# Optimization experiments

Measured on AMD Instinct MI355X. Metric: run time of the kernel, lower is better.

The kernel has to match this reference:

```python
import jax, jax.numpy as jnp
import numpy as np
from jax import lax

# Dims fixed by the module: Linear(96,24) => 16 channels * (24/4) length => per-step feature L=24
L = 24

def _conv1d(x, w, b):
    # x: (N, Cin, L), w: (Cout, Cin, K), 'same' padding for K=3
    y = lax.conv_general_dilated(x, w, window_strides=(1,), padding=[(1, 1)],
                                 dimension_numbers=("NCH", "OIH", "NCH"))
    return y + b[None, :, None]

def _maxpool2(x):
    # x: (N, C, L) -> (N, C, L//2), non-overlapping window of 2
    n, c, l = x.shape
    return x.reshape(n, c, l // 2, 2).max(axis=-1)

def setup_inputs() -> dict:
    key = jax.random.key(0)
    ks = jax.random.split(key, 11)
    S, B = 512, 256
    def u(k, shape, fan_in):
        bound = 1.0 / np.sqrt(fan_in)
        return jax.random.uniform(k, shape, jnp.float32, -bound, bound)
    return {
        "x":   jax.random.normal(ks[0], (S, B, L), jnp.float32),
        "w11": u(ks[1], (8, 1, 3), 1 * 3),   "b11": u(ks[2], (8,), 1 * 3),
        "w12": u(ks[3], (8, 8, 3), 8 * 3),   "b12": u(ks[4], (8,), 8 * 3),
        "w21": u(ks[5], (16, 8, 3), 8 * 3),  "b21": u(ks[6], (16,), 8 * 3),
        "w22": u(ks[7], (16, 16, 3), 16 * 3), "b22": u(ks[8], (16,), 16 * 3),
        "Wl":  u(ks[9], (24, 96), 96),        "bl": u(ks[10], (24,), 96),
    }

def reference(x, w11, b11, w12, b12, w21, b21, w22, b22, Wl, bl):
    # Original loops over timesteps applying the same CNN; timestep and batch
    # are independent, so fuse them into one conv batch (identical math).
    S, B, Lf = x.shape
    h = x.reshape(S * B, 1, Lf)                 # (SB, 1, 24)
    h = jax.nn.relu(_conv1d(h, w11, b11))       # (SB, 8, 24); Dropout(0.1) = identity in eval
    h = jax.nn.relu(_conv1d(h, w12, b12))       # (SB, 8, 24)
    h = _maxpool2(h)                            # (SB, 8, 12)
    h = jax.nn.relu(_conv1d(h, w21, b21))       # (SB, 16, 12); Dropout = identity in eval
    h = jax.nn.relu(_conv1d(h, w22, b22))       # (SB, 16, 12)
    h = _maxpool2(h)                            # (SB, 16, 6)
    h = h.reshape(S, B, 96)                     # torch reshape(batch, -1) per step
    return h @ Wl.T + bl                        # (S, B, 24)
```

## Files before the change

### kernel.cpp

```cpp
#include <hip/hip_runtime.h>


#define TPB 256

__launch_bounds__(TPB, 2)
__global__ void cnn_pre_lstm_kernel(
    const float* __restrict__ x,
    const float* __restrict__ w11, const float* __restrict__ b11,
    const float* __restrict__ w12, const float* __restrict__ b12,
    const float* __restrict__ w21, const float* __restrict__ b21,
    const float* __restrict__ w22, const float* __restrict__ b22,
    const float* __restrict__ Wl,  const float* __restrict__ bl,
    float* __restrict__ out)
{
    __shared__ float sA[12288];
    __shared__ float sB[6144];

    const int tid = threadIdx.x;
    const int ln  = tid & 63;
    const int wv  = __builtin_amdgcn_readfirstlane(tid >> 6);

    {
        const float* xg = x + (size_t)blockIdx.x * (64 * 24);
        #pragma unroll
        for (int k = 0; k < 6; ++k) {
            int o = tid + k * TPB;
            int s = o / 24, p = o % 24;
            sB[s * 25 + p] = xg[o];
        }
    }
    __syncthreads();

    {
        const int co0 = wv * 2;
        float wA0 = w11[co0*3+0], wA1 = w11[co0*3+1], wA2 = w11[co0*3+2];
        float wB0 = w11[(co0+1)*3+0], wB1 = w11[(co0+1)*3+1], wB2 = w11[(co0+1)*3+2];
        float bA = b11[co0], bB = b11[co0+1];

        float xm = 0.f, xc = sB[ln*25 + 0], xp;
        #pragma unroll
        for (int p = 0; p < 24; ++p) {
            xp = (p < 23) ? sB[ln*25 + p + 1] : 0.f;
            float a = fmaf(wA0, xm, fmaf(wA1, xc, fmaf(wA2, xp, bA)));
            float b = fmaf(wB0, xm, fmaf(wB1, xc, fmaf(wB2, xp, bB)));
            sA[ co0      * 1536 + p * 64 + ln] = fmaxf(a, 0.f);
            sA[(co0 + 1) * 1536 + p * 64 + ln] = fmaxf(b, 0.f);
            xm = xc; xc = xp;
        }
    }
    __syncthreads();

    {
        const int co0 = wv * 2;
        float acc[2][24];
        #pragma unroll
        for (int i = 0; i < 2; ++i) {
            float bb = b12[co0 + i];
            #pragma unroll
            for (int p = 0; p < 24; ++p) acc[i][p] = bb;
        }
        for (int ci = 0; ci < 8; ++ci) {
            float wg[2][3];
            #pragma unroll
            for (int i = 0; i < 2; ++i) {
                const float* wp = w12 + ((co0 + i) * 8 + ci) * 3;
                wg[i][0] = wp[0]; wg[i][1] = wp[1]; wg[i][2] = wp[2];
            }
            const int cb = ci * 1536 + ln;
            float xm = 0.f, xc = sA[cb], xp;
            #pragma unroll
            for (int p = 0; p < 24; ++p) {
                xp = (p < 23) ? sA[cb + (p + 1) * 64] : 0.f;
                #pragma unroll
                for (int i = 0; i < 2; ++i)
                    acc[i][p] = fmaf(wg[i][0], xm, fmaf(wg[i][1], xc, fmaf(wg[i][2], xp, acc[i][p])));
                xm = xc; xc = xp;
            }
        }
        #pragma unroll
        for (int i = 0; i < 2; ++i)
            #pragma unroll
            for (int p2 = 0; p2 < 12; ++p2)
                sB[(co0 + i) * 768 + p2 * 64 + ln] =
                    fmaxf(fmaxf(acc[i][2*p2], acc[i][2*p2+1]), 0.f);
    }
    __syncthreads();

    {
        const int co0 = wv * 4;
        float acc[4][12];
        #pragma unroll
        for (int i = 0; i < 4; ++i) {
            float bb = b21[co0 + i];
            #pragma unroll
            for (int p = 0; p < 12; ++p) acc[i][p] = bb;
        }
        for (int ci = 0; ci < 8; ++ci) {
            float wg[4][3];
            #pragma unroll
            for (int i = 0; i < 4; ++i) {
                const float* wp = w21 + ((co0 + i) * 8 + ci) * 3;
                wg[i][0] = wp[0]; wg[i][1] = wp[1]; wg[i][2] = wp[2];
            }
            const int cb = ci * 768 + ln;
            float xm = 0.f, xc = sB[cb], xp;
            #pragma unroll
            for (int p = 0; p < 12; ++p) {
                xp = (p < 11) ? sB[cb + (p + 1) * 64] : 0.f;
                #pragma unroll
                for (int i = 0; i < 4; ++i)
                    acc[i][p] = fmaf(wg[i][0], xm, fmaf(wg[i][1], xc, fmaf(wg[i][2], xp, acc[i][p])));
                xm = xc; xc = xp;
            }
        }
        #pragma unroll
        for (int i = 0; i < 4; ++i)
            #pragma unroll
            for (int p = 0; p < 12; ++p)
                sA[(co0 + i) * 768 + p * 64 + ln] = fmaxf(acc[i][p], 0.f);
    }
    __syncthreads();

    {
        const int co0 = wv * 4;
        float acc[4][12];
        #pragma unroll
        for (int i = 0; i < 4; ++i) {
            float bb = b22[co0 + i];
            #pragma unroll
            for (int p = 0; p < 12; ++p) acc[i][p] = bb;
        }
        for (int ci = 0; ci < 16; ++ci) {
            float wg[4][3];
            #pragma unroll
            for (int i = 0; i < 4; ++i) {
                const float* wp = w22 + ((co0 + i) * 16 + ci) * 3;
                wg[i][0] = wp[0]; wg[i][1] = wp[1]; wg[i][2] = wp[2];
            }
            const int cb = ci * 768 + ln;
            float xm = 0.f, xc = sA[cb], xp;
            #pragma unroll
            for (int p = 0; p < 12; ++p) {
                xp = (p < 11) ? sA[cb + (p + 1) * 64] : 0.f;
                #pragma unroll
                for (int i = 0; i < 4; ++i)
                    acc[i][p] = fmaf(wg[i][0], xm, fmaf(wg[i][1], xc, fmaf(wg[i][2], xp, acc[i][p])));
                xm = xc; xc = xp;
            }
        }
        #pragma unroll
        for (int i = 0; i < 4; ++i)
            #pragma unroll
            for (int p2 = 0; p2 < 6; ++p2)
                sB[(co0 + i) * 384 + p2 * 64 + ln] =
                    fmaxf(fmaxf(acc[i][2*p2], acc[i][2*p2+1]), 0.f);
    }
    __syncthreads();

    {
        const int j0 = wv * 6;
        float acc6[6];
        #pragma unroll
        for (int i = 0; i < 6; ++i) acc6[i] = bl[j0 + i];
        for (int c = 0; c < 16; ++c) {
            #pragma unroll
            for (int p = 0; p < 6; ++p) {
                float v = sB[c * 384 + p * 64 + ln];
                const int f = c * 6 + p;
                #pragma unroll
                for (int i = 0; i < 6; ++i)
                    acc6[i] = fmaf(Wl[(j0 + i) * 96 + f], v, acc6[i]);
            }
        }
        #pragma unroll
        for (int i = 0; i < 6; ++i)
            sA[ln * 24 + j0 + i] = acc6[i];
    }
    __syncthreads();

    {
        float* og = out + (size_t)blockIdx.x * (64 * 24);
        #pragma unroll
        for (int k = 0; k < 6; ++k) {
            int o = tid + k * TPB;
            og[o] = sA[o];
        }
    }
}

extern "C" void kernel_launch(void* const* d_in, const int* in_sizes, int n_in,
                              void* d_out, int out_size, void* d_ws, size_t ws_size,
                              hipStream_t stream) {
    const float* x   = (const float*)d_in[0];
    const float* w11 = (const float*)d_in[1];
    const float* b11 = (const float*)d_in[2];
    const float* w12 = (const float*)d_in[3];
    const float* b12 = (const float*)d_in[4];
    const float* w21 = (const float*)d_in[5];
    const float* b21 = (const float*)d_in[6];
    const float* w22 = (const float*)d_in[7];
    const float* b22 = (const float*)d_in[8];
    const float* Wl  = (const float*)d_in[9];
    const float* bl  = (const float*)d_in[10];
    float* out = (float*)d_out;

    const int n_samples = in_sizes[0] / 24;
    const int blocks = n_samples / 64;

    hipLaunchKernelGGL(cnn_pre_lstm_kernel, dim3(blocks), dim3(TPB), 0, stream,
                       x, w11, b11, w12, b12, w21, b21, w22, b22, Wl, bl, out);
}
```

Measured before the change: 163.6 us.

## Use 512-thread blocks with one output channel per wave and padded output staging

Doubles the block to 8 waves, so each wave computes half as many output channels per conv stage and half as many linear outputs. This raises parallelism and cuts per-thread register and accumulator pressure, and the launch bound now asks for 4 blocks per CU. The output staging buffer is padded to a stride of 25 to avoid LDS bank conflicts on the final write. In exchange each wave now reloads the shared input rows for fewer outputs, which adds LDS read traffic, and the large per-block LDS footprint may limit how many blocks actually fit on a CU.

New measurement: 164.1 us. No clear change (+0.3%).

```diff
diff --git a/kernel.cpp b/kernel.cpp
--- a/kernel.cpp
+++ b/kernel.cpp
@@ -1,9 +1,9 @@
 #include <hip/hip_runtime.h>
 
 
-#define TPB 256
-
-__launch_bounds__(TPB, 2)
+#define TPB 512
+
+__launch_bounds__(TPB, 4)
 __global__ void cnn_pre_lstm_kernel(
     const float* __restrict__ x,
     const float* __restrict__ w11, const float* __restrict__ b11,
@@ -23,7 +23,7 @@
     {
         const float* xg = x + (size_t)blockIdx.x * (64 * 24);
         #pragma unroll
-        for (int k = 0; k < 6; ++k) {
+        for (int k = 0; k < 3; ++k) {
             int o = tid + k * TPB;
             int s = o / 24, p = o % 24;
             sB[s * 25 + p] = xg[o];
@@ -32,45 +32,69 @@
     __syncthreads();
 
     {
-        const int co0 = wv * 2;
-        float wA0 = w11[co0*3+0], wA1 = w11[co0*3+1], wA2 = w11[co0*3+2];
-        float wB0 = w11[(co0+1)*3+0], wB1 = w11[(co0+1)*3+1], wB2 = w11[(co0+1)*3+2];
-        float bA = b11[co0], bB = b11[co0+1];
+        const int co = wv;
+        float w0 = w11[co*3+0], w1 = w11[co*3+1], w2 = w11[co*3+2];
+        float bb = b11[co];
 
         float xm = 0.f, xc = sB[ln*25 + 0], xp;
         #pragma unroll
         for (int p = 0; p < 24; ++p) {
             xp = (p < 23) ? sB[ln*25 + p + 1] : 0.f;
-            float a = fmaf(wA0, xm, fmaf(wA1, xc, fmaf(wA2, xp, bA)));
-            float b = fmaf(wB0, xm, fmaf(wB1, xc, fmaf(wB2, xp, bB)));
-            sA[ co0      * 1536 + p * 64 + ln] = fmaxf(a, 0.f);
-            sA[(co0 + 1) * 1536 + p * 64 + ln] = fmaxf(b, 0.f);
+            float a = fmaf(w0, xm, fmaf(w1, xc, fmaf(w2, xp, bb)));
+            sA[co * 1536 + p * 64 + ln] = fmaxf(a, 0.f);
             xm = xc; xc = xp;
         }
     }
     __syncthreads();
 
     {
+        const int co = wv;
+        float acc[24];
+        {
+            float bb = b12[co];
+            #pragma unroll
+            for (int p = 0; p < 24; ++p) acc[p] = bb;
+        }
+        for (int ci = 0; ci < 8; ++ci) {
+            const float* wp = w12 + (co * 8 + ci) * 3;
+            float w0 = wp[0], w1 = wp[1], w2 = wp[2];
+            const int cb = ci * 1536 + ln;
+            float xm = 0.f, xc = sA[cb], xp;
+            #pragma unroll
+            for (int p = 0; p < 24; ++p) {
+                xp = (p < 23) ? sA[cb + (p + 1) * 64] : 0.f;
+                acc[p] = fmaf(w0, xm, fmaf(w1, xc, fmaf(w2, xp, acc[p])));
+                xm = xc; xc = xp;
+            }
+        }
+        #pragma unroll
+        for (int q = 0; q < 12; ++q)
+            sB[co * 768 + q * 64 + ln] =
+                fmaxf(fmaxf(acc[2*q], acc[2*q+1]), 0.f);
+    }
+    __syncthreads();
+
+    {
         const int co0 = wv * 2;
-        float acc[2][24];
+        float acc[2][12];
         #pragma unroll
         for (int i = 0; i < 2; ++i) {
-            float bb = b12[co0 + i];
-            #pragma unroll
-            for (int p = 0; p < 24; ++p) acc[i][p] = bb;
+            float bb = b21[co0 + i];
+            #pragma unroll
+            for (int p = 0; p < 12; ++p) acc[i][p] = bb;
         }
         for (int ci = 0; ci < 8; ++ci) {
             float wg[2][3];
             #pragma unroll
             for (int i = 0; i < 2; ++i) {
-                const float* wp = w12 + ((co0 + i) * 8 + ci) * 3;
+                const float* wp = w21 + ((co0 + i) * 8 + ci) * 3;
                 wg[i][0] = wp[0]; wg[i][1] = wp[1]; wg[i][2] = wp[2];
             }
-            const int cb = ci * 1536 + ln;
-            float xm = 0.f, xc = sA[cb], xp;
-            #pragma unroll
-            for (int p = 0; p < 24; ++p) {
-                xp = (p < 23) ? sA[cb + (p + 1) * 64] : 0.f;
+            const int cb = ci * 768 + ln;
+            float xm = 0.f, xc = sB[cb], xp;
+            #pragma unroll
+            for (int p = 0; p < 12; ++p) {
+                xp = (p < 11) ? sB[cb + (p + 1) * 64] : 0.f;
                 #pragma unroll
                 for (int i = 0; i < 2; ++i)
                     acc[i][p] = fmaf(wg[i][0], xm, fmaf(wg[i][1], xc, fmaf(wg[i][2], xp, acc[i][p])));
@@ -80,60 +104,24 @@
         #pragma unroll
         for (int i = 0; i < 2; ++i)
             #pragma unroll
-            for (int p2 = 0; p2 < 12; ++p2)
-                sB[(co0 + i) * 768 + p2 * 64 + ln] =
-                    fmaxf(fmaxf(acc[i][2*p2], acc[i][2*p2+1]), 0.f);
-    }
-    __syncthreads();
-
-    {
-        const int co0 = wv * 4;
-        float acc[4][12];
-        #pragma unroll
-        for (int i = 0; i < 4; ++i) {
-            float bb = b21[co0 + i];
-            #pragma unroll
-            for (int p = 0; p < 12; ++p) acc[i][p] = bb;
-        }
-        for (int ci = 0; ci < 8; ++ci) {
-            float wg[4][3];
-            #pragma unroll
-            for (int i = 0; i < 4; ++i) {
-                const float* wp = w21 + ((co0 + i) * 8 + ci) * 3;
-                wg[i][0] = wp[0]; wg[i][1] = wp[1]; wg[i][2] = wp[2];
-            }
-            const int cb = ci * 768 + ln;
-            float xm = 0.f, xc = sB[cb], xp;
-            #pragma unroll
-            for (int p = 0; p < 12; ++p) {
-                xp = (p < 11) ? sB[cb + (p + 1) * 64] : 0.f;
-                #pragma unroll
-                for (int i = 0; i < 4; ++i)
-                    acc[i][p] = fmaf(wg[i][0], xm, fmaf(wg[i][1], xc, fmaf(wg[i][2], xp, acc[i][p])));
-                xm = xc; xc = xp;
-            }
-        }
-        #pragma unroll
-        for (int i = 0; i < 4; ++i)
-            #pragma unroll
             for (int p = 0; p < 12; ++p)
                 sA[(co0 + i) * 768 + p * 64 + ln] = fmaxf(acc[i][p], 0.f);
     }
     __syncthreads();
 
     {
-        const int co0 = wv * 4;
-        float acc[4][12];
-        #pragma unroll
-        for (int i = 0; i < 4; ++i) {
+        const int co0 = wv * 2;
+        float acc[2][12];
+        #pragma unroll
+        for (int i = 0; i < 2; ++i) {
             float bb = b22[co0 + i];
             #pragma unroll
             for (int p = 0; p < 12; ++p) acc[i][p] = bb;
         }
         for (int ci = 0; ci < 16; ++ci) {
-            float wg[4][3];
-            #pragma unroll
-            for (int i = 0; i < 4; ++i) {
+            float wg[2][3];
+            #pragma unroll
+            for (int i = 0; i < 2; ++i) {
                 const float* wp = w22 + ((co0 + i) * 16 + ci) * 3;
                 wg[i][0] = wp[0]; wg[i][1] = wp[1]; wg[i][2] = wp[2];
             }
@@ -143,47 +131,48 @@
             for (int p = 0; p < 12; ++p) {
                 xp = (p < 11) ? sA[cb + (p + 1) * 64] : 0.f;
                 #pragma unroll
-                for (int i = 0; i < 4; ++i)
+                for (int i = 0; i < 2; ++i)
                     acc[i][p] = fmaf(wg[i][0], xm, fmaf(wg[i][1], xc, fmaf(wg[i][2], xp, acc[i][p])));
                 xm = xc; xc = xp;
             }
         }
         #pragma unroll
-        for (int i = 0; i < 4; ++i)
-            #pragma unroll
-            for (int p2 = 0; p2 < 6; ++p2)
-                sB[(co0 + i) * 384 + p2 * 64 + ln] =
-                    fmaxf(fmaxf(acc[i][2*p2], acc[i][2*p2+1]), 0.f);
-    }
-    __syncthreads();
-
-    {
-        const int j0 = wv * 6;
-        float acc6[6];
-        #pragma unroll
-        for (int i = 0; i < 6; ++i) acc6[i] = bl[j0 + i];
+        for (int i = 0; i < 2; ++i)
+            #pragma unroll
+            for (int q = 0; q < 6; ++q)
+                sB[(co0 + i) * 384 + q * 64 + ln] =
+                    fmaxf(fmaxf(acc[i][2*q], acc[i][2*q+1]), 0.f);
+    }
+    __syncthreads();
+
+    {
+        const int j0 = wv * 3;
+        float acc3[3];
+        #pragma unroll
+        for (int i = 0; i < 3; ++i) acc3[i] = bl[j0 + i];
         for (int c = 0; c < 16; ++c) {
             #pragma unroll
             for (int p = 0; p < 6; ++p) {
                 float v = sB[c * 384 + p * 64 + ln];
                 const int f = c * 6 + p;
                 #pragma unroll
-                for (int i = 0; i < 6; ++i)
-                    acc6[i] = fmaf(Wl[(j0 + i) * 96 + f], v, acc6[i]);
-            }
-        }
-        #pragma unroll
-        for (int i = 0; i < 6; ++i)
-            sA[ln * 24 + j0 + i] = acc6[i];
+                for (int i = 0; i < 3; ++i)
+                    acc3[i] = fmaf(Wl[(j0 + i) * 96 + f], v, acc3[i]);
+            }
+        }
+        #pragma unroll
+        for (int i = 0; i < 3; ++i)
+            sA[ln * 25 + j0 + i] = acc3[i];
     }
     __syncthreads();
 
     {
         float* og = out + (size_t)blockIdx.x * (64 * 24);
         #pragma unroll
-        for (int k = 0; k < 6; ++k) {
+        for (int k = 0; k < 3; ++k) {
             int o = tid + k * TPB;
-            og[o] = sA[o];
+            int s = o / 24, j = o % 24;
+            og[o] = sA[s * 25 + j];
         }
     }
 }
```

## Fuse conv1 and conv2 per wave over spatial slices with halo recompute

Applied to the files above, without the earlier changes.

Each wave now owns a spatial slice of positions for all channels instead of a subset of channels over all positions, so conv11 and conv12 are fused in registers and one barrier and shared-memory round trip disappear. Halos are recomputed or read with masks at slice edges. Padded strides (29, 97, 25) are used in shared memory to avoid bank conflicts. Register pressure rises (8x8 and 8x6 arrays, full unrolling), which could hurt occupancy, and the halo work duplicates some conv1 arithmetic.

New measurement: 194.7 us. 19.1% more time.

```diff
diff --git a/kernel.cpp b/kernel.cpp
--- a/kernel.cpp
+++ b/kernel.cpp
@@ -13,177 +13,177 @@
     const float* __restrict__ Wl,  const float* __restrict__ bl,
     float* __restrict__ out)
 {
-    __shared__ float sA[12288];
-    __shared__ float sB[6144];
+    __shared__ float bufA[12288];
+    __shared__ float bufB[6208];
 
     const int tid = threadIdx.x;
     const int ln  = tid & 63;
     const int wv  = __builtin_amdgcn_readfirstlane(tid >> 6);
 
     {
-        const float* xg = x + (size_t)blockIdx.x * (64 * 24);
+        const float* xg = x + (size_t)blockIdx.x * 1536;
         #pragma unroll
         for (int k = 0; k < 6; ++k) {
             int o = tid + k * TPB;
             int s = o / 24, p = o % 24;
-            sB[s * 25 + p] = xg[o];
-        }
-    }
-    __syncthreads();
-
-    {
-        const int co0 = wv * 2;
-        float wA0 = w11[co0*3+0], wA1 = w11[co0*3+1], wA2 = w11[co0*3+2];
-        float wB0 = w11[(co0+1)*3+0], wB1 = w11[(co0+1)*3+1], wB2 = w11[(co0+1)*3+2];
-        float bA = b11[co0], bB = b11[co0+1];
-
-        float xm = 0.f, xc = sB[ln*25 + 0], xp;
-        #pragma unroll
-        for (int p = 0; p < 24; ++p) {
-            xp = (p < 23) ? sB[ln*25 + p + 1] : 0.f;
-            float a = fmaf(wA0, xm, fmaf(wA1, xc, fmaf(wA2, xp, bA)));
-            float b = fmaf(wB0, xm, fmaf(wB1, xc, fmaf(wB2, xp, bB)));
-            sA[ co0      * 1536 + p * 64 + ln] = fmaxf(a, 0.f);
-            sA[(co0 + 1) * 1536 + p * 64 + ln] = fmaxf(b, 0.f);
-            xm = xc; xc = xp;
-        }
-    }
-    __syncthreads();
-
-    {
-        const int co0 = wv * 2;
-        float acc[2][24];
-        #pragma unroll
-        for (int i = 0; i < 2; ++i) {
-            float bb = b12[co0 + i];
-            #pragma unroll
-            for (int p = 0; p < 24; ++p) acc[i][p] = bb;
-        }
+            bufA[s * 29 + 2 + p] = xg[o];
+        }
+        #pragma unroll
+        for (int z = tid; z < 320; z += TPB) {
+            int s = z / 5, which = z % 5;
+            int idx = (which < 2) ? which : (24 + which);
+            bufA[s * 29 + idx] = 0.f;
+        }
+    }
+    __syncthreads();
+
+    const float mLo = (wv == 0) ? 0.f : 1.f;
+    const float mHi = (wv == 3) ? 0.f : 1.f;
+
+    {
+        const int p0 = wv * 6;
+        float xw[10];
+        #pragma unroll
+        for (int i = 0; i < 10; ++i) xw[i] = bufA[ln * 29 + p0 + i];
+
+        float h1w[8][8];
+        #pragma unroll
+        for (int c = 0; c < 8; ++c) {
+            float w0 = w11[c*3+0], w1 = w11[c*3+1], w2 = w11[c*3+2], bb = b11[c];
+            #pragma unroll
+            for (int i = 0; i < 8; ++i)
+                h1w[c][i] = fmaxf(fmaf(w0, xw[i], fmaf(w1, xw[i+1], fmaf(w2, xw[i+2], bb))), 0.f);
+            h1w[c][0] *= mLo;
+            h1w[c][7] *= mHi;
+        }
+
+        #pragma unroll
+        for (int co = 0; co < 8; ++co) {
+            float acc[6];
+            float bb = b12[co];
+            #pragma unroll
+            for (int p = 0; p < 6; ++p) acc[p] = bb;
+            #pragma unroll
+            for (int ci = 0; ci < 8; ++ci) {
+                const float* wp = w12 + (co*8 + ci)*3;
+                float w0 = wp[0], w1 = wp[1], w2 = wp[2];
+                #pragma unroll
+                for (int p = 0; p < 6; ++p)
+                    acc[p] = fmaf(w0, h1w[ci][p], fmaf(w1, h1w[ci][p+1], fmaf(w2, h1w[ci][p+2], acc[p])));
+            }
+            #pragma unroll
+            for (int q = 0; q < 3; ++q)
+                bufB[ln*97 + co*12 + 3*wv + q] =
+                    fmaxf(fmaxf(acc[2*q], acc[2*q+1]), 0.f);
+        }
+    }
+    __syncthreads();
+
+    {
+        const int p0 = wv * 3;
+        const int pL = (wv == 0) ? 0  : (p0 - 1);
+        const int pR = (wv == 3) ? 11 : (p0 + 3);
+
+        float h2w[8][5];
+        #pragma unroll
         for (int ci = 0; ci < 8; ++ci) {
-            float wg[2][3];
-            #pragma unroll
-            for (int i = 0; i < 2; ++i) {
-                const float* wp = w12 + ((co0 + i) * 8 + ci) * 3;
-                wg[i][0] = wp[0]; wg[i][1] = wp[1]; wg[i][2] = wp[2];
-            }
-            const int cb = ci * 1536 + ln;
-            float xm = 0.f, xc = sA[cb], xp;
-            #pragma unroll
-            for (int p = 0; p < 24; ++p) {
-                xp = (p < 23) ? sA[cb + (p + 1) * 64] : 0.f;
+            h2w[ci][0] = bufB[ln*97 + ci*12 + pL] * mLo;
+            #pragma unroll
+            for (int i = 1; i < 4; ++i)
+                h2w[ci][i] = bufB[ln*97 + ci*12 + p0 - 1 + i];
+            h2w[ci][4] = bufB[ln*97 + ci*12 + pR] * mHi;
+        }
+
+        #pragma unroll
+        for (int co = 0; co < 16; ++co) {
+            float a0 = b21[co], a1 = a0, a2 = a0;
+            #pragma unroll
+            for (int ci = 0; ci < 8; ++ci) {
+                const float* wp = w21 + (co*8 + ci)*3;
+                float w0 = wp[0], w1 = wp[1], w2 = wp[2];
+                a0 = fmaf(w0, h2w[ci][0], fmaf(w1, h2w[ci][1], fmaf(w2, h2w[ci][2], a0)));
+                a1 = fmaf(w0, h2w[ci][1], fmaf(w1, h2w[ci][2], fmaf(w2, h2w[ci][3], a1)));
+                a2 = fmaf(w0, h2w[ci][2], fmaf(w1, h2w[ci][3], fmaf(w2, h2w[ci][4], a2)));
+            }
+            bufA[co*768 + (p0 + 0)*64 + ln] = fmaxf(a0, 0.f);
+            bufA[co*768 + (p0 + 1)*64 + ln] = fmaxf(a1, 0.f);
+            bufA[co*768 + (p0 + 2)*64 + ln] = fmaxf(a2, 0.f);
+        }
+    }
+    __syncthreads();
+
+    {
+        const int wc = wv & 1, wq = wv >> 1;
+        const int co0 = 8 * wc, p0 = 6 * wq;
+        const float mL4 = (wq == 0) ? 0.f : 1.f;
+        const float mR4 = (wq == 1) ? 0.f : 1.f;
+        const int pL = (wq == 0) ? 0  : (p0 - 1);
+        const int pR = (wq == 1) ? 11 : (p0 + 6);
+
+        float acc[8][6];
+        #pragma unroll
+        for (int i = 0; i < 8; ++i) {
+            float bb = b22[co0 + i];
+            #pragma unroll
+            for (int p = 0; p < 6; ++p) acc[i][p] = bb;
+        }
+
+        #pragma unroll
+        for (int ci = 0; ci < 16; ++ci) {
+            float h3w[8];
+            h3w[0] = bufA[ci*768 + pL*64 + ln] * mL4;
+            #pragma unroll
+            for (int i = 1; i < 7; ++i)
+                h3w[i] = bufA[ci*768 + (p0 - 1 + i)*64 + ln];
+            h3w[7] = bufA[ci*768 + pR*64 + ln] * mR4;
+
+            #pragma unroll
+            for (int io = 0; io < 8; ++io) {
+                const float* wp = w22 + ((co0 + io)*16 + ci)*3;
+                float w0 = wp[0], w1 = wp[1], w2 = wp[2];
                 #pragma unroll
-                for (int i = 0; i < 2; ++i)
-                    acc[i][p] = fmaf(wg[i][0], xm, fmaf(wg[i][1], xc, fmaf(wg[i][2], xp, acc[i][p])));
-                xm = xc; xc = xp;
-            }
-        }
-        #pragma unroll
-        for (int i = 0; i < 2; ++i)
-            #pragma unroll
-            for (int p2 = 0; p2 < 12; ++p2)
-                sB[(co0 + i) * 768 + p2 * 64 + ln] =
-                    fmaxf(fmaxf(acc[i][2*p2], acc[i][2*p2+1]), 0.f);
-    }
-    __syncthreads();
-
-    {
-        const int co0 = wv * 4;
-        float acc[4][12];
-        #pragma unroll
-        for (int i = 0; i < 4; ++i) {
-            float bb = b21[co0 + i];
-            #pragma unroll
-            for (int p = 0; p < 12; ++p) acc[i][p] = bb;
-        }
-        for (int ci = 0; ci < 8; ++ci) {
-            float wg[4][3];
-            #pragma unroll
-            for (int i = 0; i < 4; ++i) {
-                const float* wp = w21 + ((co0 + i) * 8 + ci) * 3;
-                wg[i][0] = wp[0]; wg[i][1] = wp[1]; wg[i][2] = wp[2];
-            }
-            const int cb = ci * 768 + ln;
-            float xm = 0.f, xc = sB[cb], xp;
-            #pragma unroll
-            for (int p = 0; p < 12; ++p) {
-                xp = (p < 11) ? sB[cb + (p + 1) * 64] : 0.f;
-                #pragma unroll
-                for (int i = 0; i < 4; ++i)
-                    acc[i][p] = fmaf(wg[i][0], xm, fmaf(wg[i][1], xc, fmaf(wg[i][2], xp, acc[i][p])));
-                xm = xc; xc = xp;
-            }
-        }
-        #pragma unroll
-        for (int i = 0; i < 4; ++i)
-            #pragma unroll
-            for (int p = 0; p < 12; ++p)
-                sA[(co0 + i) * 768 + p * 64 + ln] = fmaxf(acc[i][p], 0.f);
-    }
-    __syncthreads();
-
-    {
-        const int co0 = wv * 4;
-        float acc[4][12];
-        #pragma unroll
-        for (int i = 0; i < 4; ++i) {
-            float bb = b22[co0 + i];
-            #pragma unroll
-            for (int p = 0; p < 12; ++p) acc[i][p] = bb;
-        }
-        for (int ci = 0; ci < 16; ++ci) {
-            float wg[4][3];
-            #pragma unroll
-            for (int i = 0; i < 4; ++i) {
-                const float* wp = w22 + ((co0 + i) * 16 + ci) * 3;
-                wg[i][0] = wp[0]; wg[i][1] = wp[1]; wg[i][2] = wp[2];
-            }
-            const int cb = ci * 768 + ln;
-            float xm = 0.f, xc = sA[cb], xp;
-            #pragma unroll
-            for (int p = 0; p < 12; ++p) {
-                xp = (p < 11) ? sA[cb + (p + 1) * 64] : 0.f;
-                #pragma unroll
-                for (int i = 0; i < 4; ++i)
-                    acc[i][p] = fmaf(wg[i][0], xm, fmaf(wg[i][1], xc, fmaf(wg[i][2], xp, acc[i][p])));
-                xm = xc; xc = xp;
-            }
-        }
-        #pragma unroll
-        for (int i = 0; i < 4; ++i)
-            #pragma unroll
-            for (int p2 = 0; p2 < 6; ++p2)
-                sB[(co0 + i) * 384 + p2 * 64 + ln] =
-                    fmaxf(fmaxf(acc[i][2*p2], acc[i][2*p2+1]), 0.f);
+                for (int p = 0; p < 6; ++p)
+                    acc[io][p] = fmaf(w0, h3w[p], fmaf(w1, h3w[p+1], fmaf(w2, h3w[p+2], acc[io][p])));
+            }
+        }
+
+        #pragma unroll
+        for (int io = 0; io < 8; ++io)
+            #pragma unroll
+            for (int q = 0; q < 3; ++q)
+                bufB[ln*97 + (co0 + io)*6 + 3*wq + q] =
+                    fmaxf(fmaxf(acc[io][2*q], acc[io][2*q+1]), 0.f);
     }
     __syncthreads();
 
     {
         const int j0 = wv * 6;
-        float acc6[6];
-        #pragma unroll
-        for (int i = 0; i < 6; ++i) acc6[i] = bl[j0 + i];
-        for (int c = 0; c < 16; ++c) {
+        float y[6];
+        #pragma unroll
+        for (int i = 0; i < 6; ++i) y[i] = bl[j0 + i];
+        #pragma unroll
+        for (int c = 0; c < 16; ++c)
             #pragma unroll
             for (int p = 0; p < 6; ++p) {
-                float v = sB[c * 384 + p * 64 + ln];
-                const int f = c * 6 + p;
+                float v = bufB[ln*97 + c*6 + p];
+                const int f = c*6 + p;
                 #pragma unroll
                 for (int i = 0; i < 6; ++i)
-                    acc6[i] = fmaf(Wl[(j0 + i) * 96 + f], v, acc6[i]);
-            }
-        }
+                    y[i] = fmaf(Wl[(j0 + i)*96 + f], v, y[i]);
+            }
         #pragma unroll
         for (int i = 0; i < 6; ++i)
-            sA[ln * 24 + j0 + i] = acc6[i];
-    }
-    __syncthreads();
-
-    {
-        float* og = out + (size_t)blockIdx.x * (64 * 24);
+            bufA[ln*25 + j0 + i] = y[i];
+    }
+    __syncthreads();
+
+    {
+        float* og = out + (size_t)blockIdx.x * 1536;
         #pragma unroll
         for (int k = 0; k < 6; ++k) {
             int o = tid + k * TPB;
-            og[o] = sA[o];
+            int s = o / 24, j = o % 24;
+            og[o] = bufA[s*25 + j];
         }
     }
 }
```

## Stage weights in LDS and store conv intermediates as fp16

Applied to the files above, without the earlier changes.

Copies all conv and linear weights and biases into shared memory once per block and reads them from there. Stores the conv1 and conv3 activations in shared memory as half precision to shrink the LDS footprint. Preloads the 96 pooled features into registers and uses float4 weight reads for the final linear layer, with a padded output tile. This aims to cut global scalar weight loads and LDS pressure, at the cost of fp16 rounding of activations and more register use.

Result: slower. 174.4 us (+6.7%).

```diff
diff --git a/kernel.cpp b/kernel.cpp
--- a/kernel.cpp
+++ b/kernel.cpp
@@ -1,7 +1,19 @@
 #include <hip/hip_runtime.h>
+#include <hip/hip_fp16.h>
 
 
 #define TPB 256
+
+#define oW11 0
+#define oW12 24
+#define oW21 216
+#define oW22 600
+#define oWl  1368
+#define oB11 3672
+#define oB12 3680
+#define oB21 3688
+#define oB22 3704
+#define oBl  3720
 
 __launch_bounds__(TPB, 2)
 __global__ void cnn_pre_lstm_kernel(
@@ -13,38 +25,49 @@
     const float* __restrict__ Wl,  const float* __restrict__ bl,
     float* __restrict__ out)
 {
-    __shared__ float sA[12288];
-    __shared__ float sB[6144];
+    __shared__ __align__(16) __half hA[12288];
+    __shared__ __align__(16) float  fB[6144];
+    __shared__ __align__(16) float  sW[3744];
 
     const int tid = threadIdx.x;
     const int ln  = tid & 63;
     const int wv  = __builtin_amdgcn_readfirstlane(tid >> 6);
 
-    {
-        const float* xg = x + (size_t)blockIdx.x * (64 * 24);
+    if (tid < 48)  ((float4*)(sW + oW12))[tid] = ((const float4*)w12)[tid];
+    if (tid < 96)  ((float4*)(sW + oW21))[tid] = ((const float4*)w21)[tid];
+    if (tid < 192) ((float4*)(sW + oW22))[tid] = ((const float4*)w22)[tid];
+    #pragma unroll
+    for (int i = tid; i < 576; i += TPB)
+        ((float4*)(sW + oWl))[i] = ((const float4*)Wl)[i];
+    if (tid < 24) sW[oW11 + tid] = w11[tid];
+    if (tid < 8)  { sW[oB11 + tid] = b11[tid]; sW[oB12 + tid] = b12[tid]; }
+    if (tid < 16) { sW[oB21 + tid] = b21[tid]; sW[oB22 + tid] = b22[tid]; }
+    if (tid < 24) sW[oBl + tid] = bl[tid];
+    {
+        const float* xg = x + (size_t)blockIdx.x * 1536;
         #pragma unroll
         for (int k = 0; k < 6; ++k) {
             int o = tid + k * TPB;
             int s = o / 24, p = o % 24;
-            sB[s * 25 + p] = xg[o];
+            fB[s * 25 + p] = xg[o];
         }
     }
     __syncthreads();
 
     {
         const int co0 = wv * 2;
-        float wA0 = w11[co0*3+0], wA1 = w11[co0*3+1], wA2 = w11[co0*3+2];
-        float wB0 = w11[(co0+1)*3+0], wB1 = w11[(co0+1)*3+1], wB2 = w11[(co0+1)*3+2];
-        float bA = b11[co0], bB = b11[co0+1];
-
-        float xm = 0.f, xc = sB[ln*25 + 0], xp;
+        float wA0 = sW[oW11+co0*3+0], wA1 = sW[oW11+co0*3+1], wA2 = sW[oW11+co0*3+2];
+        float wB0 = sW[oW11+co0*3+3], wB1 = sW[oW11+co0*3+4], wB2 = sW[oW11+co0*3+5];
+        float bA = sW[oB11+co0], bB = sW[oB11+co0+1];
+
+        float xm = 0.f, xc = fB[ln*25 + 0], xp;
         #pragma unroll
         for (int p = 0; p < 24; ++p) {
-            xp = (p < 23) ? sB[ln*25 + p + 1] : 0.f;
+            xp = (p < 23) ? fB[ln*25 + p + 1] : 0.f;
             float a = fmaf(wA0, xm, fmaf(wA1, xc, fmaf(wA2, xp, bA)));
             float b = fmaf(wB0, xm, fmaf(wB1, xc, fmaf(wB2, xp, bB)));
-            sA[ co0      * 1536 + p * 64 + ln] = fmaxf(a, 0.f);
-            sA[(co0 + 1) * 1536 + p * 64 + ln] = fmaxf(b, 0.f);
+            hA[ co0      * 1536 + p * 64 + ln] = __float2half(fmaxf(a, 0.f));
+            hA[(co0 + 1) * 1536 + p * 64 + ln] = __float2half(fmaxf(b, 0.f));
             xm = xc; xc = xp;
         }
     }
@@ -53,24 +76,23 @@
     {
         const int co0 = wv * 2;
         float acc[2][24];
-        #pragma unroll
-        for (int i = 0; i < 2; ++i) {
-            float bb = b12[co0 + i];
-            #pragma unroll
-            for (int p = 0; p < 24; ++p) acc[i][p] = bb;
+        {
+            float bb0 = sW[oB12+co0], bb1 = sW[oB12+co0+1];
+            #pragma unroll
+            for (int p = 0; p < 24; ++p) { acc[0][p] = bb0; acc[1][p] = bb1; }
         }
         for (int ci = 0; ci < 8; ++ci) {
             float wg[2][3];
             #pragma unroll
-            for (int i = 0; i < 2; ++i) {
-                const float* wp = w12 + ((co0 + i) * 8 + ci) * 3;
-                wg[i][0] = wp[0]; wg[i][1] = wp[1]; wg[i][2] = wp[2];
-            }
+            for (int i = 0; i < 2; ++i)
+                #pragma unroll
+                for (int k = 0; k < 3; ++k)
+                    wg[i][k] = sW[oW12 + (co0 + i)*24 + ci*3 + k];
             const int cb = ci * 1536 + ln;
-            float xm = 0.f, xc = sA[cb], xp;
+            float xm = 0.f, xc = __half2float(hA[cb]), xp;
             #pragma unroll
             for (int p = 0; p < 24; ++p) {
-                xp = (p < 23) ? sA[cb + (p + 1) * 64] : 0.f;
+                xp = (p < 23) ? __half2float(hA[cb + (p + 1) * 64]) : 0.f;
                 #pragma unroll
                 for (int i = 0; i < 2; ++i)
                     acc[i][p] = fmaf(wg[i][0], xm, fmaf(wg[i][1], xc, fmaf(wg[i][2], xp, acc[i][p])));
@@ -80,9 +102,9 @@
         #pragma unroll
         for (int i = 0; i < 2; ++i)
             #pragma unroll
-            for (int p2 = 0; p2 < 12; ++p2)
-                sB[(co0 + i) * 768 + p2 * 64 + ln] =
-                    fmaxf(fmaxf(acc[i][2*p2], acc[i][2*p2+1]), 0.f);
+            for (int q = 0; q < 12; ++q)
+                fB[(co0 + i) * 768 + q * 64 + ln] =
+                    fmaxf(fmaxf(acc[i][2*q], acc[i][2*q+1]), 0.f);
     }
     __syncthreads();
 
@@ -91,22 +113,22 @@
         float acc[4][12];
         #pragma unroll
         for (int i = 0; i < 4; ++i) {
-            float bb = b21[co0 + i];
+            float bb = sW[oB21 + co0 + i];
             #pragma unroll
             for (int p = 0; p < 12; ++p) acc[i][p] = bb;
         }
         for (int ci = 0; ci < 8; ++ci) {
             float wg[4][3];
             #pragma unroll
-            for (int i = 0; i < 4; ++i) {
-                const float* wp = w21 + ((co0 + i) * 8 + ci) * 3;
-                wg[i][0] = wp[0]; wg[i][1] = wp[1]; wg[i][2] = wp[2];
-            }
+            for (int i = 0; i < 4; ++i)
+                #pragma unroll
+                for (int k = 0; k < 3; ++k)
+                    wg[i][k] = sW[oW21 + (co0 + i)*24 + ci*3 + k];
             const int cb = ci * 768 + ln;
-            float xm = 0.f, xc = sB[cb], xp;
+            float xm = 0.f, xc = fB[cb], xp;
             #pragma unroll
             for (int p = 0; p < 12; ++p) {
-                xp = (p < 11) ? sB[cb + (p + 1) * 64] : 0.f;
+                xp = (p < 11) ? fB[cb + (p + 1) * 64] : 0.f;
                 #pragma unroll
                 for (int i = 0; i < 4; ++i)
                     acc[i][p] = fmaf(wg[i][0], xm, fmaf(wg[i][1], xc, fmaf(wg[i][2], xp, acc[i][p])));
@@ -117,7 +139,7 @@
         for (int i = 0; i < 4; ++i)
             #pragma unroll
             for (int p = 0; p < 12; ++p)
-                sA[(co0 + i) * 768 + p * 64 + ln] = fmaxf(acc[i][p], 0.f);
+                hA[(co0 + i) * 768 + p * 64 + ln] = __float2half(fmaxf(acc[i][p], 0.f));
     }
     __syncthreads();
 
@@ -126,22 +148,22 @@
         float acc[4][12];
         #pragma unroll
         for (int i = 0; i < 4; ++i) {
-            float bb = b22[co0 + i];
+            float bb = sW[oB22 + co0 + i];
             #pragma unroll
             for (int p = 0; p < 12; ++p) acc[i][p] = bb;
         }
         for (int ci = 0; ci < 16; ++ci) {
             float wg[4][3];
             #pragma unroll
-            for (int i = 0; i < 4; ++i) {
-                const float* wp = w22 + ((co0 + i) * 16 + ci) * 3;
-                wg[i][0] = wp[0]; wg[i][1] = wp[1]; wg[i][2] = wp[2];
-            }
+            for (int i = 0; i < 4; ++i)
+                #pragma unroll
+                for (int k = 0; k < 3; ++k)
+                    wg[i][k] = sW[oW22 + (co0 + i)*48 + ci*3 + k];
             const int cb = ci * 768 + ln;
-            float xm = 0.f, xc = sA[cb], xp;
+            float xm = 0.f, xc = __half2float(hA[cb]), xp;
             #pragma unroll
             for (int p = 0; p < 12; ++p) {
-                xp = (p < 11) ? sA[cb + (p + 1) * 64] : 0.f;
+                xp = (p < 11) ? __half2float(hA[cb + (p + 1) * 64]) : 0.f;
                 #pragma unroll
                 for (int i = 0; i < 4; ++i)
                     acc[i][p] = fmaf(wg[i][0], xm, fmaf(wg[i][1], xc, fmaf(wg[i][2], xp, acc[i][p])));
@@ -151,39 +173,49 @@
         #pragma unroll
         for (int i = 0; i < 4; ++i)
             #pragma unroll
-            for (int p2 = 0; p2 < 6; ++p2)
-                sB[(co0 + i) * 384 + p2 * 64 + ln] =
-                    fmaxf(fmaxf(acc[i][2*p2], acc[i][2*p2+1]), 0.f);
+            for (int q = 0; q < 6; ++q)
+                fB[(co0 + i) * 384 + q * 64 + ln] =
+                    fmaxf(fmaxf(acc[i][2*q], acc[i][2*q+1]), 0.f);
     }
     __syncthreads();
 
     {
         const int j0 = wv * 6;
+        float v[96];
+        #pragma unroll
+        for (int c = 0; c < 16; ++c)
+            #pragma unroll
+            for (int p = 0; p < 6; ++p)
+                v[c*6 + p] = fB[c * 384 + p * 64 + ln];
+
         float acc6[6];
         #pragma unroll
-        for (int i = 0; i < 6; ++i) acc6[i] = bl[j0 + i];
-        for (int c = 0; c < 16; ++c) {
-            #pragma unroll
-            for (int p = 0; p < 6; ++p) {
-                float v = sB[c * 384 + p * 64 + ln];
-                const int f = c * 6 + p;
-                #pragma unroll
-                for (int i = 0; i < 6; ++i)
-                    acc6[i] = fmaf(Wl[(j0 + i) * 96 + f], v, acc6[i]);
+        for (int i = 0; i < 6; ++i) acc6[i] = sW[oBl + j0 + i];
+
+        float* sOutF = (float*)hA;
+        #pragma unroll
+        for (int q = 0; q < 24; ++q) {
+            #pragma unroll
+            for (int i = 0; i < 6; ++i) {
+                float4 w4 = ((const float4*)(sW + oWl + (j0 + i) * 96))[q];
+                acc6[i] = fmaf(w4.x, v[q*4+0], fmaf(w4.y, v[q*4+1],
+                          fmaf(w4.z, v[q*4+2], fmaf(w4.w, v[q*4+3], acc6[i]))));
             }
         }
         #pragma unroll
         for (int i = 0; i < 6; ++i)
-            sA[ln * 24 + j0 + i] = acc6[i];
-    }
-    __syncthreads();
-
-    {
-        float* og = out + (size_t)blockIdx.x * (64 * 24);
+            sOutF[ln * 25 + j0 + i] = acc6[i];
+    }
+    __syncthreads();
+
+    {
+        const float* sOutF = (const float*)hA;
+        float* og = out + (size_t)blockIdx.x * 1536;
         #pragma unroll
         for (int k = 0; k < 6; ++k) {
             int o = tid + k * TPB;
-            og[o] = sA[o];
+            int s = o / 24, j = o % 24;
+            og[o] = sOutF[s * 25 + j];
         }
     }
 }
```
